# Optimization experiments

Hardware: AMD Instinct MI355X
Metric: run time of the kernel (lower is better)

Reference implementation:

```python
import jax, jax.numpy as jnp
import numpy as np

B, C, H, W = 8, 512, 32, 32
S, E = 77, 768
NH = 8
HD = C // NH
HID = 4 * C
EPS2D = 1e-6
EPS_QK = 1.1920929e-07  # torch nn.RMSNorm default eps = fp32 machine eps


def rotate_half(x):
    p = x.reshape(*x.shape[:-1], -1, 2)
    p = jnp.stack([-p[..., 1], p[..., 0]], axis=-1)
    return p.reshape(x.shape)


def rope_1d(x):
    # x: [B, NH, S, HD] -- standard 1D RoPE over the sequence axis
    d = x.shape[-1]
    inv_freq = 1.0 / (10000.0 ** (jnp.arange(0, d, 2, dtype=jnp.float32) / d))
    ang = jnp.arange(x.shape[-2], dtype=jnp.float32)[:, None] * inv_freq[None, :]  # [S, HD/2]
    cos = jnp.repeat(jnp.cos(ang), 2, axis=-1)
    sin = jnp.repeat(jnp.sin(ang), 2, axis=-1)
    return x * cos + rotate_half(x) * sin


def rope_2d(x, freqs, h, w):
    # x: [B, NH, H*W, HD]; freqs: [HD/2, 2] learned (theta_y, theta_x)
    gy, gx = jnp.meshgrid(jnp.arange(h, dtype=jnp.float32), jnp.arange(w, dtype=jnp.float32), indexing='ij')
    ang = gy.reshape(-1)[:, None] * freqs[None, :, 0] + gx.reshape(-1)[:, None] * freqs[None, :, 1]  # [HW, HD/2]
    cos = jnp.repeat(jnp.cos(ang), 2, axis=-1)
    sin = jnp.repeat(jnp.sin(ang), 2, axis=-1)
    return x * cos + rotate_half(x) * sin


def rmsnorm_last(x, wgt, eps):
    return x * jax.lax.rsqrt(jnp.mean(x * x, axis=-1, keepdims=True) + eps) * wgt


def rmsnorm_2d(x, wgt):
    # x: [B,C,H,W], RMS over channel dim (dim=1)
    return x * jax.lax.rsqrt(jnp.mean(x * x, axis=1, keepdims=True) + EPS2D) * wgt[None, :, None, None]


def setup_inputs() -> dict:
    key = jax.random.key(0)
    ks = jax.random.split(key, 12)

    def n(k, shp, s=0.02):
        return jax.random.normal(k, shp, jnp.float32) * s

    return {
        'x': jax.random.normal(ks[0], (B, C, H, W), jnp.float32),
        'cond_seq': jax.random.normal(ks[1], (B, S, E), jnp.float32),
        'final_emb': jax.random.normal(ks[2], (B, E), jnp.float32),
        'mod_w': n(ks[3], (E, 6 * C)),
        'mod_b': jnp.zeros((6 * C,), jnp.float32),
        'norm1_scale': jnp.ones((C,), jnp.float32),
        'norm2_scale': jnp.ones((C,), jnp.float32),
        'qkv_s_w': n(ks[4], (3 * C, C)),
        'qkv_c_w': n(ks[5], (3 * C, E)),
        'rope_freqs': jax.random.normal(ks[6], (HD // 2, 2), jnp.float32),
        'qn_w': jnp.ones((HD,), jnp.float32),
        'kn_w': jnp.ones((HD,), jnp.float32),
        'out_w': n(ks[7], (C, C)),
        'out_b': jnp.zeros((C,), jnp.float32),
        'mlp_w1': n(ks[8], (HID, C)),
        'mlp_b1': jnp.zeros((HID,), jnp.float32),
        'mlp_w2': n(ks[9], (C, HID)),
        'mlp_b2': jnp.zeros((C,), jnp.float32),
    }


def reference(x, cond_seq, final_emb, mod_w, mod_b, norm1_scale, norm2_scale,
              qkv_s_w, qkv_c_w, rope_freqs, qn_w, kn_w, out_w, out_b,
              mlp_w1, mlp_b1, mlp_w2, mlp_b2):
    b, c, h, w = x.shape
    hw = h * w
    # adaLN modulation (Modulation: SiLU -> Linear -> 6 chunks)
    mod = jax.nn.silu(final_emb) @ mod_w + mod_b  # [B, 6C]
    sh1, sc1, g1, sh2, sc2, g2 = jnp.split(mod, 6, axis=-1)

    def modulate(z, shift, scale):
        return z * (1.0 + scale[:, :, None, None]) + shift[:, :, None, None]

    h_mod = modulate(rmsnorm_2d(x, norm1_scale), sh1, sc1)

    # --- FusedAttentionBlock: dual-stream (spatial + conditional) attention ---
    hm = h_mod.reshape(b, c, hw)
    qkv_s = jnp.einsum('bcn,oc->bon', hm, qkv_s_w)  # 1x1 conv, [B,3C,HW]
    q_s, k_s, v_s = jnp.split(qkv_s, 3, axis=1)

    def to_heads(t):  # [B,C,HW] -> [B,NH,HW,HD] (head-major channel layout)
        return t.reshape(b, NH, HD, hw).transpose(0, 1, 3, 2)

    q_s, k_s, v_s = to_heads(q_s), to_heads(k_s), to_heads(v_s)

    qkv_c = jnp.einsum('bse,oe->bso', cond_seq, qkv_c_w)
    qkv_c = qkv_c.reshape(b, -1, 3, NH, HD).transpose(2, 0, 3, 1, 4)
    q_c, k_c, v_c = qkv_c[0], qkv_c[1], qkv_c[2]  # [B,NH,S,HD]

    q = jnp.concatenate([rope_2d(q_s, rope_freqs, h, w), rope_1d(q_c)], axis=2)
    k = jnp.concatenate([rope_2d(k_s, rope_freqs, h, w), rope_1d(k_c)], axis=2)
    v = jnp.concatenate([v_s, v_c], axis=2)

    q = rmsnorm_last(q, qn_w, EPS_QK)
    k = rmsnorm_last(k, kn_w, EPS_QK)

    scale = 1.0 / (HD ** 0.5)
    logits = jnp.einsum('bhqd,bhkd->bhqk', q, k) * scale
    attn = jax.nn.softmax(logits, axis=-1)
    o = jnp.einsum('bhqk,bhkd->bhqd', attn, v)[:, :, :hw, :]  # spatial stream only
    o = o.transpose(0, 2, 1, 3).reshape(b, hw, c)
    o = jnp.einsum('bnc,oc->bno', o, out_w) + out_b
    attn_out = o.transpose(0, 2, 1).reshape(b, c, h, w)

    x = x + g1[:, :, None, None] * attn_out

    # --- MLP (1x1 convs, tanh-approx GELU) ---
    h2 = modulate(rmsnorm_2d(x, norm2_scale), sh2, sc2)
    m = jnp.einsum('bchw,oc->bohw', h2, mlp_w1) + mlp_b1[None, :, None, None]
    m = jax.nn.gelu(m, approximate=True)
    m = jnp.einsum('bchw,oc->bohw', m, mlp_w2) + mlp_b2[None, :, None, None]
    return x + g2[:, :, None, None] * m
```

## Files before the change

### kernel.cpp

```cpp
#include <hip/hip_runtime.h>

constexpr int BATCH = 8, CH = 512, HWN = 1024, SEQ = 77, EMB = 768;
constexpr int NHEAD = 8, HDIM = 64, HIDDEN = 2048, TTOT = 1101;
constexpr int VSTRIDE = 1152;

typedef short bhalf8 __attribute__((ext_vector_type(8)));
typedef float f32x4 __attribute__((ext_vector_type(4)));

__device__ __forceinline__ unsigned short f2bf(float f) {
    unsigned u = __builtin_bit_cast(unsigned, f);
    unsigned r = (u + 0x7fffu + ((u >> 16) & 1u)) >> 16;
    return (unsigned short)r;
}
__device__ __forceinline__ unsigned cvtpk(float a, float b) {
    unsigned r;
    asm("v_cvt_pk_bf16_f32 %0, %1, %2" : "=v"(r) : "v"(a), "v"(b));
    return r;
}
__device__ __forceinline__ float gelu_tanh(float v) {
    float c = v * v * v;
    float t = tanhf(0.7978845608028654f * (v + 0.044715f * c));
    return 0.5f * v * (1.0f + t);
}
__device__ __forceinline__ int swz(int b) { return b ^ ((b >> 3) & 0x70); }

__device__ __forceinline__ void gload16(const void* g, void* l) {
    __builtin_amdgcn_global_load_lds(
        (const __attribute__((address_space(1))) unsigned int*)g,
        (__attribute__((address_space(3))) unsigned int*)l, 16, 0, 0);
}

struct PrepArgs {
    const float* src[6];
    unsigned short* dst[6];
    int n[6];
    const float* freqs;
    float* ct;
    const float* emb;
    const float* mbias;
    float* mod;
    float* se;
};
__global__ void k_prep(PrepArgs a) {
    int y = blockIdx.y;
    int bx = blockIdx.x;
    int tid = threadIdx.x;
    if (y < 6) {
        int i = (bx * 256 + tid) * 4;
        if (i >= a.n[y]) return;
        float4 v = *(const float4*)&a.src[y][i];
        ushort4 o = {f2bf(v.x), f2bf(v.y), f2bf(v.z), f2bf(v.w)};
        *(ushort4*)&a.dst[y][i] = o;
    } else if (y == 6) {
        int i = bx * 256 + tid;
        if (i >= TTOT * 32) return;
        int t = i >> 5, j = i & 31;
        float ang;
        if (t < HWN) {
            ang = (float)(t >> 5) * a.freqs[2 * j] + (float)(t & 31) * a.freqs[2 * j + 1];
        } else {
            float inv = expf(-(float)j * (9.210340371976184f / 32.0f));
            ang = (float)(t - HWN) * inv;
        }
        a.ct[i * 2] = cosf(ang);
        a.ct[i * 2 + 1] = sinf(ang);
    } else {
        if (bx < 24) {
            int i = bx * 1024 + tid * 4;
            int j = i - (i / (6 * CH)) * (6 * CH);
            *(float4*)&a.mod[i] = *(const float4*)&a.mbias[j];
        } else if (bx >= 32 && bx < 38) {
            int i = (bx - 32) * 1024 + tid * 4;
            float4 v = *(const float4*)&a.emb[i];
            float4 o;
            o.x = v.x / (1.0f + expf(-v.x));
            o.y = v.y / (1.0f + expf(-v.y));
            o.z = v.z / (1.0f + expf(-v.z));
            o.w = v.w / (1.0f + expf(-v.w));
            *(float4*)&a.se[i] = o;
        }
    }
}

__global__ __launch_bounds__(256) void k_mod(const float* __restrict__ se,
        const float* __restrict__ w, float* __restrict__ mod) {
    int jb = blockIdx.x, b = blockIdx.y, ec = blockIdx.z;
    int j = jb * 256 + threadIdx.x;
    const float* sb = se + b * EMB + ec * 96;
    const float* wb = w + (size_t)(ec * 96) * (6 * CH) + j;
    float acc = 0.f;
    #pragma unroll 8
    for (int e = 0; e < 96; ++e) acc = fmaf(sb[e], wb[(size_t)e * (6 * CH)], acc);
    atomicAdd(&mod[b * (6 * CH) + j], acc);
}

__global__ __launch_bounds__(256) void k_rms2d_mod_t(const float* __restrict__ xin,
        const float* __restrict__ sw, const float* __restrict__ mod, int shoff, int scoff,
        unsigned short* __restrict__ outp) {
    __shared__ float part[4][64];
    __shared__ float rinv[64];
    int b = blockIdx.y;
    int n0 = blockIdx.x * 64;
    int tid = threadIdx.x;
    const float* xb = xin + (size_t)b * CH * HWN;
    {
        int n = n0 + (tid & 63);
        int cg = tid >> 6;
        float ss = 0.f;
        #pragma unroll 8
        for (int c = cg * 128; c < cg * 128 + 128; ++c) {
            float v = xb[(size_t)c * HWN + n];
            ss = fmaf(v, v, ss);
        }
        part[cg][tid & 63] = ss;
    }
    __syncthreads();
    if (tid < 64) {
        float s = part[0][tid] + part[1][tid] + part[2][tid] + part[3][tid];
        rinv[tid] = rsqrtf(s * (1.0f / CH) + 1e-6f);
    }
    __syncthreads();
    int n = n0 + (tid >> 2);
    int cq = tid & 3;
    float r = rinv[tid >> 2];
    const float* mb = mod + b * (6 * CH);
    unsigned short* orow = outp + ((size_t)(b * HWN + n)) * CH;
    for (int jc = 0; jc < 16; ++jc) {
        int c = cq * 128 + jc * 8;
        bhalf8 o;
        #pragma unroll
        for (int u = 0; u < 8; ++u) {
            int cc = c + u;
            float v = xb[(size_t)cc * HWN + n];
            float y = v * r * sw[cc] * (1.0f + mb[scoff + cc]) + mb[shoff + cc];
            o[u] = (short)f2bf(y);
        }
        *(bhalf8*)&orow[c] = o;
    }
}

template <int EPI, int BM, int BN>
__global__ __launch_bounds__(256) void k_gemm_mfma(
        const unsigned short* __restrict__ A, const unsigned short* __restrict__ Bt,
        void* __restrict__ OutV, int M, int N, int K,
        const float* __restrict__ bias, const float* __restrict__ gate,
        const float* __restrict__ res) {
    constexpr int WM = BM / 2, WN = BN / 2;
    constexpr int MI = WM / 16, NI = WN / 16;
    constexpr int CA = BM / 8, CB = BN / 8, CW = (CA + CB) / 4;
    constexpr int BUF = (BM + BN) * 128;
    constexpr unsigned WAIT_CW = (CW & 0xF) | ((CW >> 4) << 14) | (0x7 << 4) | (0xF << 8);
    constexpr unsigned WAIT_0 = (0x7 << 4) | (0xF << 8);
    __shared__ __align__(1024) char SM[3 * BUF];
    int tid = threadIdx.x;
    int w = tid >> 6, l = tid & 63, lg = l >> 4, ll = l & 15;
    int wr = w >> 1, wc = w & 1;
    int m0 = blockIdx.y * BM, n0 = blockIdx.x * BN;
    int r8 = l >> 3, c16 = (l & 7) * 16;
    f32x4 acc[MI][NI] = {};
    const char* Ac = (const char*)A;
    const char* Bc = (const char*)Bt;
    size_t rowBytes = (size_t)K * 2;
    int nt = K >> 6;

    auto stage = [&](int t, int bsel) {
        char* As = SM + bsel * BUF;
        char* Bs = As + BM * 128;
        int k0 = t * 64;
        #pragma unroll
        for (int i = 0; i < CW; ++i) {
            int c = w * CW + i;
            if (c < CA) {
                int row = c * 8 + r8;
                int off = c16 ^ ((row & 7) << 4);
                int ar = m0 + row;
                if (ar > M - 1) ar = M - 1;
                gload16(Ac + (size_t)ar * rowBytes + k0 * 2 + off, As + c * 1024);
            } else {
                int cc = c - CA;
                int row = cc * 8 + r8;
                int off = c16 ^ ((row & 7) << 4);
                gload16(Bc + (size_t)(n0 + row) * rowBytes + k0 * 2 + off, Bs + cc * 1024);
            }
        }
    };
    stage(0, 0);
    stage(1, 1);
    int cur = 0;
    for (int t = 0; t < nt; ++t) {
        if (t + 1 < nt) __builtin_amdgcn_s_waitcnt(WAIT_CW);
        else __builtin_amdgcn_s_waitcnt(WAIT_0);
        __builtin_amdgcn_s_barrier();
        __builtin_amdgcn_sched_barrier(0);
        if (t + 2 < nt) stage(t + 2, (cur + 2) % 3);
        char* As = SM + cur * BUF;
        char* Bs = As + BM * 128;
        #pragma unroll
        for (int ks = 0; ks < 2; ++ks) {
            bhalf8 af[MI], bf[NI];
            #pragma unroll
            for (int mi = 0; mi < MI; ++mi)
                af[mi] = *(const bhalf8*)(As + swz((wr * WM + mi * 16 + ll) * 128 + ks * 64 + lg * 16));
            #pragma unroll
            for (int ni = 0; ni < NI; ++ni)
                bf[ni] = *(const bhalf8*)(Bs + swz((wc * WN + ni * 16 + ll) * 128 + ks * 64 + lg * 16));
            __builtin_amdgcn_s_setprio(1);
            #pragma unroll
            for (int mi = 0; mi < MI; ++mi)
                #pragma unroll
                for (int ni = 0; ni < NI; ++ni)
                    acc[mi][ni] = __builtin_amdgcn_mfma_f32_16x16x32_bf16(af[mi], bf[ni], acc[mi][ni], 0, 0, 0);
            __builtin_amdgcn_s_setprio(0);
        }
        __builtin_amdgcn_sched_barrier(0);
        cur = (cur + 1) % 3;
    }
    if (EPI == 2) {
        unsigned short* Out = (unsigned short*)OutV;
        #pragma unroll
        for (int mi = 0; mi < MI; ++mi)
            #pragma unroll
            for (int ni = 0; ni < NI; ++ni) {
                int col = n0 + wc * WN + ni * 16 + ll;
                float bv = bias[col];
                #pragma unroll
                for (int r = 0; r < 4; ++r) {
                    int mrow = m0 + wr * WM + mi * 16 + 4 * lg + r;
                    Out[(size_t)mrow * N + col] = f2bf(gelu_tanh(acc[mi][ni][r] + bv));
                }
            }
    } else {
        float* Out = (float*)OutV;
        int bidx = m0 >> 10;
        int hw0 = m0 & 1023;
        const float* resb = res + (size_t)bidx * N * HWN;
        float* outb_ = Out + (size_t)bidx * N * HWN;
        #pragma unroll
        for (int ni = 0; ni < NI; ++ni) {
            int ch = n0 + wc * WN + ni * 16 + ll;
            float g = gate[bidx * (6 * CH) + ch];
            float bv = bias[ch];
            #pragma unroll
            for (int mi = 0; mi < MI; ++mi) {
                int t = hw0 + wr * WM + mi * 16 + 4 * lg;
                float4 r4 = *(const float4*)&resb[(size_t)ch * HWN + t];
                f32x4 a = acc[mi][ni];
                float4 o;
                o.x = r4.x + g * (a[0] + bv);
                o.y = r4.y + g * (a[1] + bv);
                o.z = r4.z + g * (a[2] + bv);
                o.w = r4.w + g * (a[3] + bv);
                *(float4*)&outb_[(size_t)ch * HWN + t] = o;
            }
        }
    }
}

template <int COND>
__global__ __launch_bounds__(256) void k_gemm_qkv(
        const unsigned short* __restrict__ A, const unsigned short* __restrict__ Bt,
        int M, int K, int nOff, const float* __restrict__ ct,
        const float* __restrict__ qn, const float* __restrict__ kn,
        unsigned short* __restrict__ qb, unsigned short* __restrict__ kb,
        unsigned short* __restrict__ vT) {
    __shared__ __align__(1024) char SMEM[34816];
    unsigned short* As = (unsigned short*)SMEM;
    unsigned short* Bs = (unsigned short*)(SMEM + 16384);
    int tid = threadIdx.x;
    int w = tid >> 6, l = tid & 63, lg = l >> 4, ll = l & 15;
    int wr = w >> 1, wc = w & 1;
    int m0 = blockIdx.y * 128, n0 = nOff + blockIdx.x * 128;
    int r8 = l >> 3, c16 = (l & 7) * 16;
    f32x4 acc[4][4] = {};
    const char* Ac = (const char*)A;
    const char* Bc = (const char*)Bt;
    size_t rowBytes = (size_t)K * 2;
    for (int k0 = 0; k0 < K; k0 += 64) {
        __syncthreads();
        #pragma unroll
        for (int i = 0; i < 8; ++i) {
            int c = w * 8 + i;
            if (c < 16) {
                int row = c * 8 + r8;
                int off = c16 ^ ((row & 7) << 4);
                int ar = m0 + row;
                if (ar > M - 1) ar = M - 1;
                gload16(Ac + (size_t)ar * rowBytes + k0 * 2 + off, (char*)As + c * 1024);
            } else {
                int cc = c - 16;
                int row = cc * 8 + r8;
                int off = c16 ^ ((row & 7) << 4);
                gload16(Bc + (size_t)(n0 + row) * rowBytes + k0 * 2 + off, (char*)Bs + cc * 1024);
            }
        }
        __syncthreads();
        #pragma unroll
        for (int ks = 0; ks < 2; ++ks) {
            bhalf8 af[4], bf[4];
            #pragma unroll
            for (int mi = 0; mi < 4; ++mi)
                af[mi] = *(const bhalf8*)((char*)As + swz((wr * 64 + mi * 16 + ll) * 128 + ks * 64 + lg * 16));
            #pragma unroll
            for (int ni = 0; ni < 4; ++ni)
                bf[ni] = *(const bhalf8*)((char*)Bs + swz((wc * 64 + ni * 16 + ll) * 128 + ks * 64 + lg * 16));
            __builtin_amdgcn_s_setprio(1);
            #pragma unroll
            for (int mi = 0; mi < 4; ++mi)
                #pragma unroll
                for (int ni = 0; ni < 4; ++ni)
                    acc[mi][ni] = __builtin_amdgcn_mfma_f32_16x16x32_bf16(af[mi], bf[ni], acc[mi][ni], 0, 0, 0);
            __builtin_amdgcn_s_setprio(0);
        }
    }
    int type = n0 >> 9;
    const float2* ct2 = (const float2*)ct;

    if (type >= 2) {
        int hd = (n0 - 1024 + wc * 64) >> 6;
        #pragma unroll
        for (int ni = 0; ni < 4; ++ni) {
            int d = ni * 16 + ll;
            #pragma unroll
            for (int mi = 0; mi < 4; ++mi) {
                int rowL = m0 + wr * 64 + mi * 16 + 4 * lg;
                if (COND == 0) {
                    int b = rowL >> 10, t = rowL & 1023;
                    uint2 pk = {cvtpk(acc[mi][ni][0], acc[mi][ni][1]),
                                cvtpk(acc[mi][ni][2], acc[mi][ni][3])};
                    *(uint2*)&vT[((size_t)(b * 8 + hd) * 64 + d) * VSTRIDE + t] = pk;
                } else {
                    #pragma unroll
                    for (int r = 0; r < 4; ++r) {
                        int row = rowL + r;
                        if (row < M) {
                            int b = row / 77, s = row - b * 77;
                            vT[((size_t)(b * 8 + hd) * 64 + d) * VSTRIDE + 1024 + s] =
                                f2bf(acc[mi][ni][r]);
                        }
                    }
                }
            }
        }
        return;
    }
    const float* wnt = (type == 0) ? qn : kn;
    float wn[4];
    int jj[4];
    #pragma unroll
    for (int ni = 0; ni < 4; ++ni) {
        wn[ni] = wnt[ni * 16 + ll];
        jj[ni] = (ni * 16 + ll) >> 1;
    }
    float sgn = (ll & 1) ? 1.f : -1.f;
    #pragma unroll
    for (int mi = 0; mi < 4; ++mi) {
        int rowL = m0 + wr * 64 + mi * 16 + 4 * lg;
        int tt[4];
        #pragma unroll
        for (int r = 0; r < 4; ++r) {
            if (COND == 0) tt[r] = (rowL + r) & 1023;
            else {
                int row = rowL + r;
                if (row > M - 1) row = M - 1;
                int b = row / 77;
                tt[r] = 1024 + (row - b * 77);
            }
        }
        #pragma unroll
        for (int ni = 0; ni < 4; ++ni) {
            f32x4 a = acc[mi][ni], p;
            #pragma unroll
            for (int r = 0; r < 4; ++r) p[r] = __shfl_xor(a[r], 1);
            #pragma unroll
            for (int r = 0; r < 4; ++r) {
                float2 cs = ct2[tt[r] * 32 + jj[ni]];
                a[r] = fmaf(sgn * p[r], cs.y, a[r] * cs.x);
            }
            acc[mi][ni] = a;
        }
        f32x4 ss = {};
        #pragma unroll
        for (int ni = 0; ni < 4; ++ni)
            #pragma unroll
            for (int r = 0; r < 4; ++r) ss[r] = fmaf(acc[mi][ni][r], acc[mi][ni][r], ss[r]);
        #pragma unroll
        for (int msk = 1; msk < 16; msk <<= 1)
            #pragma unroll
            for (int r = 0; r < 4; ++r) ss[r] += __shfl_xor(ss[r], msk);
        f32x4 ri;
        #pragma unroll
        for (int r = 0; r < 4; ++r) {
            ri[r] = rsqrtf(ss[r] * (1.0f / 64.f) + 1.1920929e-07f);
            if (type == 0) ri[r] *= 0.18033688011112042f;
        }
        #pragma unroll
        for (int ni = 0; ni < 4; ++ni)
            #pragma unroll
            for (int r = 0; r < 4; ++r) acc[mi][ni][r] *= ri[r] * wn[ni];
    }
    __syncthreads();
    unsigned short* stg = (unsigned short*)SMEM;
    #pragma unroll
    for (int mi = 0; mi < 4; ++mi)
        #pragma unroll
        for (int ni = 0; ni < 4; ++ni) {
            int colL = wc * 64 + ni * 16 + ll;
            int rowL = wr * 64 + mi * 16 + 4 * lg;
            #pragma unroll
            for (int r = 0; r < 4; ++r)
                stg[(rowL + r) * 136 + colL] = f2bf(acc[mi][ni][r]);
        }
    __syncthreads();
    int rowO = tid >> 1, half = tid & 1;
    int rowG = m0 + rowO;
    if (COND == 1 && rowG >= M) return;
    int ch0 = n0 + half * 64;
    int b, t;
    if (COND == 0) { b = rowG >> 10; t = rowG & 1023; }
    else { b = rowG / 77; t = 1024 + (rowG - b * 77); }
    unsigned short* dst;
    if (type == 0) dst = qb + ((size_t)(b * 8 + (ch0 >> 6)) * HWN + t) * 64;
    else dst = kb + ((size_t)(b * 8 + ((ch0 - 512) >> 6)) * TTOT + t) * 64;
    #pragma unroll
    for (int i = 0; i < 8; ++i)
        *(bhalf8*)&dst[i * 8] = *(const bhalf8*)&stg[rowO * 136 + half * 64 + i * 8];
}

__global__ __launch_bounds__(256) void k_attn_v8(const unsigned short* __restrict__ qb,
        const unsigned short* __restrict__ kbuf, const unsigned short* __restrict__ vT,
        unsigned short* __restrict__ ob) {
    __shared__ __align__(1024) char smc[40960];
    int f = blockIdx.x;
    int xcd = f & 7, n = f >> 3;
    int q0 = (n & 15) * 64;
    int bh = ((n >> 4) << 3) | xcd;
    int tid = threadIdx.x;
    int w = tid >> 6, l = tid & 63, lg = l >> 4, ll = l & 15;
    int r8 = l >> 3, c16 = (l & 7) * 16;
    bhalf8 qf[2];
    {
        const unsigned short* qbase = qb + ((size_t)bh * HWN + q0 + w * 16) * 64;
        #pragma unroll
        for (int ks = 0; ks < 2; ++ks)
            qf[ks] = *(const bhalf8*)&qbase[ll * 64 + ks * 32 + lg * 8];
    }
    bhalf8 onesf;
    #pragma unroll
    for (int i = 0; i < 8; ++i) onesf[i] = (short)0x3F80;
    f32x4 accO[4] = {};
    f32x4 Lacc = {};
    const char* kgl = (const char*)kbuf + (size_t)bh * TTOT * 128;
    const char* vgl = (const char*)vT + (size_t)bh * 64 * (VSTRIDE * 2);
    char* pw = smc + 32768 + w * 2048 + ll * 128;
    int pswz = (ll & 7) << 4;

    auto stage = [&](int kt, int bsel) {
        char* base = smc + bsel * 16384;
        #pragma unroll
        for (int i = 0; i < 4; ++i) {
            int c = w * 4 + i;
            if (c < 8) {
                int row = c * 8 + r8;
                int t = kt * 64 + row;
                if (t > TTOT - 1) t = TTOT - 1;
                gload16(kgl + (size_t)t * 128 + (c16 ^ ((row & 7) << 4)), base + c * 1024);
            } else {
                int row = (c - 8) * 8 + r8;
                gload16(vgl + (size_t)row * (VSTRIDE * 2) + kt * 128 + (c16 ^ ((row & 7) << 4)),
                        base + 8192 + (c - 8) * 1024);
            }
        }
    };
    stage(0, 0);
    __syncthreads();
    for (int kt = 0; kt < 18; ++kt) {
        int cur = kt & 1;
        if (kt < 17) stage(kt + 1, cur ^ 1);
        char* kl = smc + cur * 16384;
        char* vl = kl + 8192;
        f32x4 s[4] = {};
        __builtin_amdgcn_s_setprio(1);
        #pragma unroll
        for (int ks = 0; ks < 2; ++ks) {
            bhalf8 kf[4];
            #pragma unroll
            for (int k4 = 0; k4 < 4; ++k4)
                kf[k4] = *(const bhalf8*)(kl + swz((k4 * 16 + ll) * 128 + ks * 64 + lg * 16));
            #pragma unroll
            for (int k4 = 0; k4 < 4; ++k4)
                s[k4] = __builtin_amdgcn_mfma_f32_16x16x32_bf16(kf[k4], qf[ks], s[k4], 0, 0, 0);
        }
        __builtin_amdgcn_s_setprio(0);
        if (kt == 17) {
            int kb0 = kt * 64 + 4 * lg;
            #pragma unroll
            for (int k4 = 0; k4 < 4; ++k4)
                #pragma unroll
                for (int r = 0; r < 4; ++r)
                    if (kb0 + k4 * 16 + r >= TTOT) s[k4][r] = -1e30f;
        }
        #pragma unroll
        for (int k4 = 0; k4 < 4; ++k4) {
            float p0 = exp2f(s[k4][0]), p1 = exp2f(s[k4][1]);
            float p2 = exp2f(s[k4][2]), p3 = exp2f(s[k4][3]);
            uint2 pk = {cvtpk(p0, p1), cvtpk(p2, p3)};
            *(uint2*)(pw + ((k4 * 32 + lg * 8) ^ pswz)) = pk;
        }
        __builtin_amdgcn_s_setprio(1);
        #pragma unroll
        for (int ks = 0; ks < 2; ++ks) {
            bhalf8 vf[4];
            #pragma unroll
            for (int d4 = 0; d4 < 4; ++d4)
                vf[d4] = *(const bhalf8*)(vl + swz((d4 * 16 + ll) * 128 + ks * 64 + lg * 16));
            bhalf8 pf = *(const bhalf8*)(smc + 32768 + w * 2048 + swz(ll * 128 + ks * 64 + lg * 16));
            Lacc = __builtin_amdgcn_mfma_f32_16x16x32_bf16(onesf, pf, Lacc, 0, 0, 0);
            #pragma unroll
            for (int d4 = 0; d4 < 4; ++d4)
                accO[d4] = __builtin_amdgcn_mfma_f32_16x16x32_bf16(vf[d4], pf, accO[d4], 0, 0, 0);
        }
        __builtin_amdgcn_s_setprio(0);
        __syncthreads();
    }
    {
        float inv = 1.0f / Lacc[0];
        int orow = w * 16 + ll;
        char* po = smc + orow * 128;
        int oswz = (orow & 7) << 4;
        #pragma unroll
        for (int d4 = 0; d4 < 4; ++d4) {
            uint2 pk = {cvtpk(accO[d4][0] * inv, accO[d4][1] * inv),
                        cvtpk(accO[d4][2] * inv, accO[d4][3] * inv)};
            *(uint2*)(po + ((d4 * 32 + lg * 8) ^ oswz)) = pk;
        }
    }
    __syncthreads();
    int b = bh >> 3, h = bh & 7;
    int row = tid >> 2, seg = tid & 3;
    bhalf8 v0 = *(const bhalf8*)(smc + swz(row * 128 + seg * 32));
    bhalf8 v1 = *(const bhalf8*)(smc + swz(row * 128 + seg * 32 + 16));
    unsigned short* dst = ob + ((size_t)(b * HWN + q0 + row)) * CH + h * 64 + seg * 16;
    *(bhalf8*)&dst[0] = v0;
    *(bhalf8*)&dst[8] = v1;
}

extern "C" void kernel_launch(void* const* d_in, const int* in_sizes, int n_in,
                              void* d_out, int out_size, void* d_ws, size_t ws_size,
                              hipStream_t stream) {
    const float* x     = (const float*)d_in[0];
    const float* cond  = (const float*)d_in[1];
    const float* femb  = (const float*)d_in[2];
    const float* mod_w = (const float*)d_in[3];
    const float* mod_b = (const float*)d_in[4];
    const float* n1s   = (const float*)d_in[5];
    const float* n2s   = (const float*)d_in[6];
    const float* qkvsw = (const float*)d_in[7];
    const float* qkvcw = (const float*)d_in[8];
    const float* ropef = (const float*)d_in[9];
    const float* qn    = (const float*)d_in[10];
    const float* kn    = (const float*)d_in[11];
    const float* outw  = (const float*)d_in[12];
    const float* outb  = (const float*)d_in[13];
    const float* w1    = (const float*)d_in[14];
    const float* b1    = (const float*)d_in[15];
    const float* w2    = (const float*)d_in[16];
    const float* b2    = (const float*)d_in[17];
    float* out = (float*)d_out;
    char* W = (char*)d_ws;

    unsigned short* wqs_b = (unsigned short*)(W + 0);
    unsigned short* wqc_b = (unsigned short*)(W + 1572864);
    unsigned short* wo_b  = (unsigned short*)(W + 3932160);
    unsigned short* w1_b  = (unsigned short*)(W + 4456448);
    unsigned short* w2_b  = (unsigned short*)(W + 6553600);
    unsigned short* condb = (unsigned short*)(W + 8650752);
    float* mod            = (float*)(W + 9596928);
    float* ct             = (float*)(W + 9695232);
    unsigned short* hmod  = (unsigned short*)(W + 9977088);
    unsigned short* obuf  = hmod;
    unsigned short* qbuf  = (unsigned short*)(W + 18365696);
    unsigned short* kbuf  = (unsigned short*)(W + 26754304);
    unsigned short* vTb   = (unsigned short*)(W + 35772672);
    unsigned short* h2    = vTb;
    unsigned short* mbuf  = (unsigned short*)(W + 45209856);
    float* x1             = (float*)(W + 78764288);
    float* sebuf          = (float*)(W + 45209920);

    PrepArgs pa;
    pa.src[0] = qkvsw; pa.dst[0] = wqs_b; pa.n[0] = 1536 * 512;
    pa.src[1] = qkvcw; pa.dst[1] = wqc_b; pa.n[1] = 1536 * 768;
    pa.src[2] = outw;  pa.dst[2] = wo_b;  pa.n[2] = 512 * 512;
    pa.src[3] = w1;    pa.dst[3] = w1_b;  pa.n[3] = 2048 * 512;
    pa.src[4] = w2;    pa.dst[4] = w2_b;  pa.n[4] = 512 * 2048;
    pa.src[5] = cond;  pa.dst[5] = condb; pa.n[5] = 616 * 768;
    pa.freqs = ropef; pa.ct = ct;
    pa.emb = femb; pa.mbias = mod_b; pa.mod = mod; pa.se = sebuf;
    k_prep<<<dim3(1152, 8), 256, 0, stream>>>(pa);
    k_mod<<<dim3(12, 8, 8), 256, 0, stream>>>(sebuf, mod_w, mod);

    k_rms2d_mod_t<<<dim3(16, BATCH), 256, 0, stream>>>(x, n1s, mod, 0, 512, hmod);
    k_gemm_qkv<0><<<dim3(12, 64), 256, 0, stream>>>(hmod, wqs_b, 8192, 512, 0,
                                                    ct, qn, kn, qbuf, kbuf, vTb);
    k_gemm_qkv<1><<<dim3(8, 5), 256, 0, stream>>>(condb, wqc_b, 616, 768, 512,
                                                  ct, qn, kn, qbuf, kbuf, vTb);
    k_attn_v8<<<dim3(1024), 256, 0, stream>>>(qbuf, kbuf, vTb, obuf);
    k_gemm_mfma<1, 128, 64><<<dim3(8, 64), 256, 0, stream>>>(
        obuf, wo_b, x1, 8192, 512, 512, outb, mod + 2 * 512, x);
    k_rms2d_mod_t<<<dim3(16, BATCH), 256, 0, stream>>>(x1, n2s, mod, 3 * 512, 4 * 512, h2);
    k_gemm_mfma<2, 64, 128><<<dim3(16, 128), 256, 0, stream>>>(
        h2, w1_b, mbuf, 8192, 2048, 512, b1, nullptr, nullptr);
    k_gemm_mfma<1, 128, 64><<<dim3(8, 64), 256, 0, stream>>>(
        mbuf, w2_b, out, 8192, 512, 2048, b2, mod + 5 * 512, x1);
}
```

Measured before the change: 269.5 us.

## Merge QKV launches, simplify GEMM pipeline to double buffer, faster GELU, larger MLP1 tile

Several changes at once. The triple-buffered GEMM with fine-grained waitcnt is replaced by a simpler double-buffered loop that uses __syncthreads. The spatial and conditioning QKV GEMMs are merged into one launch with a flattened grid. The tanh GELU is rewritten in an exp2/rcp form that is algebraically equivalent. The MLP1 GEMM tile grows to 128x128. Together these aim to cut launch count and transcendental cost and to improve tile reuse, but the simpler pipeline may expose more global-load latency.

```diff
diff --git a/kernel.cpp b/kernel.cpp
--- a/kernel.cpp
+++ b/kernel.cpp
@@ -17,10 +17,13 @@
     asm("v_cvt_pk_bf16_f32 %0, %1, %2" : "=v"(r) : "v"(a), "v"(b));
     return r;
 }
-__device__ __forceinline__ float gelu_tanh(float v) {
+__device__ __forceinline__ float gelu_fast(float v) {
     float c = v * v * v;
-    float t = tanhf(0.7978845608028654f * (v + 0.044715f * c));
-    return 0.5f * v * (1.0f + t);
+    float z = fmaf(v, 2.3022082f, c * 0.10294324f);
+    float e = exp2f(z) + 1.0f;
+    float r;
+    asm("v_rcp_f32 %0, %1" : "=v"(r) : "v"(e));
+    return v - v * r;
 }
 __device__ __forceinline__ int swz(int b) { return b ^ ((b >> 3) & 0x70); }
 
@@ -149,9 +152,7 @@
     constexpr int MI = WM / 16, NI = WN / 16;
     constexpr int CA = BM / 8, CB = BN / 8, CW = (CA + CB) / 4;
     constexpr int BUF = (BM + BN) * 128;
-    constexpr unsigned WAIT_CW = (CW & 0xF) | ((CW >> 4) << 14) | (0x7 << 4) | (0xF << 8);
-    constexpr unsigned WAIT_0 = (0x7 << 4) | (0xF << 8);
-    __shared__ __align__(1024) char SM[3 * BUF];
+    __shared__ __align__(1024) char SM[2 * BUF];
     int tid = threadIdx.x;
     int w = tid >> 6, l = tid & 63, lg = l >> 4, ll = l & 15;
     int wr = w >> 1, wc = w & 1;
@@ -185,14 +186,10 @@
         }
     };
     stage(0, 0);
-    stage(1, 1);
+    __syncthreads();
     int cur = 0;
     for (int t = 0; t < nt; ++t) {
-        if (t + 1 < nt) __builtin_amdgcn_s_waitcnt(WAIT_CW);
-        else __builtin_amdgcn_s_waitcnt(WAIT_0);
-        __builtin_amdgcn_s_barrier();
-        __builtin_amdgcn_sched_barrier(0);
-        if (t + 2 < nt) stage(t + 2, (cur + 2) % 3);
+        if (t + 1 < nt) stage(t + 1, cur ^ 1);
         char* As = SM + cur * BUF;
         char* Bs = As + BM * 128;
         #pragma unroll
@@ -212,8 +209,8 @@
                     acc[mi][ni] = __builtin_amdgcn_mfma_f32_16x16x32_bf16(af[mi], bf[ni], acc[mi][ni], 0, 0, 0);
             __builtin_amdgcn_s_setprio(0);
         }
-        __builtin_amdgcn_sched_barrier(0);
-        cur = (cur + 1) % 3;
+        __syncthreads();
+        cur ^= 1;
     }
     if (EPI == 2) {
         unsigned short* Out = (unsigned short*)OutV;
@@ -226,7 +223,7 @@
                 #pragma unroll
                 for (int r = 0; r < 4; ++r) {
                     int mrow = m0 + wr * WM + mi * 16 + 4 * lg + r;
-                    Out[(size_t)mrow * N + col] = f2bf(gelu_tanh(acc[mi][ni][r] + bv));
+                    Out[(size_t)mrow * N + col] = f2bf(gelu_fast(acc[mi][ni][r] + bv));
                 }
             }
     } else {
@@ -256,24 +253,34 @@
     }
 }
 
-template <int COND>
 __global__ __launch_bounds__(256) void k_gemm_qkv(
-        const unsigned short* __restrict__ A, const unsigned short* __restrict__ Bt,
-        int M, int K, int nOff, const float* __restrict__ ct,
-        const float* __restrict__ qn, const float* __restrict__ kn,
-        unsigned short* __restrict__ qb, unsigned short* __restrict__ kb,
-        unsigned short* __restrict__ vT) {
+        const unsigned short* __restrict__ Asp, const unsigned short* __restrict__ Bsp,
+        const unsigned short* __restrict__ Acn, const unsigned short* __restrict__ Bcn,
+        const float* __restrict__ ct, const float* __restrict__ qn,
+        const float* __restrict__ kn, unsigned short* __restrict__ qb,
+        unsigned short* __restrict__ kb, unsigned short* __restrict__ vT) {
     __shared__ __align__(1024) char SMEM[34816];
     unsigned short* As = (unsigned short*)SMEM;
     unsigned short* Bs = (unsigned short*)(SMEM + 16384);
+    int fid = blockIdx.x;
+    bool cond = fid >= 768;
+    int m0, n0, M, K;
+    const char *Ac, *Bc;
+    if (!cond) {
+        m0 = (fid / 12) * 128; n0 = (fid % 12) * 128;
+        M = 8192; K = 512;
+        Ac = (const char*)Asp; Bc = (const char*)Bsp;
+    } else {
+        int g = fid - 768;
+        m0 = (g >> 3) * 128; n0 = 512 + (g & 7) * 128;
+        M = 616; K = 768;
+        Ac = (const char*)Acn; Bc = (const char*)Bcn;
+    }
     int tid = threadIdx.x;
     int w = tid >> 6, l = tid & 63, lg = l >> 4, ll = l & 15;
     int wr = w >> 1, wc = w & 1;
-    int m0 = blockIdx.y * 128, n0 = nOff + blockIdx.x * 128;
     int r8 = l >> 3, c16 = (l & 7) * 16;
     f32x4 acc[4][4] = {};
-    const char* Ac = (const char*)A;
-    const char* Bc = (const char*)Bt;
     size_t rowBytes = (size_t)K * 2;
     for (int k0 = 0; k0 < K; k0 += 64) {
         __syncthreads();
@@ -323,7 +330,7 @@
             #pragma unroll
             for (int mi = 0; mi < 4; ++mi) {
                 int rowL = m0 + wr * 64 + mi * 16 + 4 * lg;
-                if (COND == 0) {
+                if (!cond) {
                     int b = rowL >> 10, t = rowL & 1023;
                     uint2 pk = {cvtpk(acc[mi][ni][0], acc[mi][ni][1]),
                                 cvtpk(acc[mi][ni][2], acc[mi][ni][3])};
@@ -332,7 +339,7 @@
                     #pragma unroll
                     for (int r = 0; r < 4; ++r) {
                         int row = rowL + r;
-                        if (row < M) {
+                        if (row < 616) {
                             int b = row / 77, s = row - b * 77;
                             vT[((size_t)(b * 8 + hd) * 64 + d) * VSTRIDE + 1024 + s] =
                                 f2bf(acc[mi][ni][r]);
@@ -358,10 +365,10 @@
         int tt[4];
         #pragma unroll
         for (int r = 0; r < 4; ++r) {
-            if (COND == 0) tt[r] = (rowL + r) & 1023;
+            if (!cond) tt[r] = (rowL + r) & 1023;
             else {
                 int row = rowL + r;
-                if (row > M - 1) row = M - 1;
+                if (row > 615) row = 615;
                 int b = row / 77;
                 tt[r] = 1024 + (row - b * 77);
             }
@@ -413,10 +420,10 @@
     __syncthreads();
     int rowO = tid >> 1, half = tid & 1;
     int rowG = m0 + rowO;
-    if (COND == 1 && rowG >= M) return;
+    if (cond && rowG >= 616) return;
     int ch0 = n0 + half * 64;
     int b, t;
-    if (COND == 0) { b = rowG >> 10; t = rowG & 1023; }
+    if (!cond) { b = rowG >> 10; t = rowG & 1023; }
     else { b = rowG / 77; t = 1024 + (rowG - b * 77); }
     unsigned short* dst;
     if (type == 0) dst = qb + ((size_t)(b * 8 + (ch0 >> 6)) * HWN + t) * 64;
@@ -599,15 +606,13 @@
     k_mod<<<dim3(12, 8, 8), 256, 0, stream>>>(sebuf, mod_w, mod);
 
     k_rms2d_mod_t<<<dim3(16, BATCH), 256, 0, stream>>>(x, n1s, mod, 0, 512, hmod);
-    k_gemm_qkv<0><<<dim3(12, 64), 256, 0, stream>>>(hmod, wqs_b, 8192, 512, 0,
-                                                    ct, qn, kn, qbuf, kbuf, vTb);
-    k_gemm_qkv<1><<<dim3(8, 5), 256, 0, stream>>>(condb, wqc_b, 616, 768, 512,
-                                                  ct, qn, kn, qbuf, kbuf, vTb);
+    k_gemm_qkv<<<dim3(808), 256, 0, stream>>>(hmod, wqs_b, condb, wqc_b,
+                                              ct, qn, kn, qbuf, kbuf, vTb);
     k_attn_v8<<<dim3(1024), 256, 0, stream>>>(qbuf, kbuf, vTb, obuf);
     k_gemm_mfma<1, 128, 64><<<dim3(8, 64), 256, 0, stream>>>(
         obuf, wo_b, x1, 8192, 512, 512, outb, mod + 2 * 512, x);
     k_rms2d_mod_t<<<dim3(16, BATCH), 256, 0, stream>>>(x1, n2s, mod, 3 * 512, 4 * 512, h2);
-    k_gemm_mfma<2, 64, 128><<<dim3(16, 128), 256, 0, stream>>>(
+    k_gemm_mfma<2, 128, 128><<<dim3(16, 64), 256, 0, stream>>>(
         h2, w1_b, mbuf, 8192, 2048, 512, b1, nullptr, nullptr);
     k_gemm_mfma<1, 128, 64><<<dim3(8, 64), 256, 0, stream>>>(
         mbuf, w2_b, out, 8192, 512, 2048, b2, mod + 5 * 512, x1);
```

Measured after the change: 256.8 us. -4.7%, faster.
